# Kernel optimization log

Hardware: AMD Instinct MI355X
Metric: run time of the kernel (lower is better)

The kernel has to match this reference:

```python
import jax, jax.numpy as jnp
import numpy as np

B, S, D, DEPTH = 2, 2048, 1024, 4
NUM_LEAVES = 2 ** DEPTH          # 16
NUM_DEC = NUM_LEAVES - 1         # 15


def setup_inputs() -> dict:
    key = jax.random.key(0)
    k1, k2, k3, k4, k5 = jax.random.split(key, 5)
    scale = 1.0 / np.sqrt(D)
    return {
        "x": jax.random.normal(k1, (B, S, D), dtype=jnp.float32),
        "dec_w": jax.random.normal(k2, (NUM_DEC, D), dtype=jnp.float32) * scale,
        "dec_b": jax.random.normal(k3, (NUM_DEC,), dtype=jnp.float32) * scale,
        "leaf_w": jax.random.normal(k4, (NUM_LEAVES, D, D), dtype=jnp.float32) * scale,  # [leaf, out, in] (torch Linear layout)
        "leaf_b": jax.random.normal(k5, (NUM_LEAVES, D), dtype=jnp.float32) * scale,
    }


def reference(x, dec_w, dec_b, leaf_w, leaf_b):
    num_leaves = leaf_w.shape[0]
    num_dec = num_leaves - 1
    # All decision-node sigmoids in one batched GEMM: [B,S,num_dec]
    dec = jax.nn.sigmoid(jnp.einsum("bsd,nd->bsn", x, dec_w) + dec_b)
    # Faithful to the original: each tree slot is multiplied exactly once by its
    # direct parent's decision (left child: p, right child: 1-p).
    leaf_idx = np.arange(num_dec, 2 * num_leaves - 1)      # slots holding leaf probs
    parent = (leaf_idx - 1) // 2                           # [num_leaves]
    is_left = (leaf_idx % 2 == 1)                          # [num_leaves]
    dec_p = dec[..., parent]                               # [B,S,num_leaves]
    leaf_probs = jnp.where(jnp.asarray(is_left), dec_p, 1.0 - dec_p)
    # All leaf MLPs as one batched GEMM: [B,S,L,D]
    leaf_out = jnp.einsum("bsd,lod->bslo", x, leaf_w) + leaf_b
    # Probability-weighted sum over leaves -> [B,S,D]
    return jnp.einsum("bslo,bsl->bso", leaf_out, leaf_probs)
```

## Files before the change

### kernel.cpp

```cpp
#include <hip/hip_runtime.h>
#include <stdint.h>


#define M_TOK 4096
#define DDIM  1024
#define KFLAT 9216

typedef __bf16 bf16x8 __attribute__((ext_vector_type(8)));
typedef float  f32x4  __attribute__((ext_vector_type(4)));
typedef unsigned short u16x4 __attribute__((ext_vector_type(4)));
typedef unsigned short u16x8 __attribute__((ext_vector_type(8)));

#define GLB(p) ((const __attribute__((address_space(1))) void*)(p))
#define LDS(p) ((__attribute__((address_space(3))) void*)(p))

__device__ __forceinline__ unsigned short f2bf(float f) {
    union { float f; uint32_t u; } v; v.f = f;
    uint32_t u = v.u;
    return (unsigned short)((u + 0x7fffu + ((u >> 16) & 1u)) >> 16);
}

__device__ __forceinline__ bf16x8 asbf(f32x4 v) {
    bf16x8 r; __builtin_memcpy(&r, &v, 16); return r;
}

template<int OFF>
__device__ __forceinline__ f32x4 dsr(uint32_t a) {
    f32x4 r;
    asm volatile("ds_read_b128 %0, %1 offset:%c2" : "=v"(r) : "v"(a), "i"(OFF));
    return r;
}

__global__ __launch_bounds__(256) void prep_dec_kernel(
    const float* __restrict__ x, const float* __restrict__ dec_w,
    const float* __restrict__ dec_b, const float* __restrict__ lw,
    const float* __restrict__ lb, unsigned short* __restrict__ wp,
    float* __restrict__ bw, unsigned short* __restrict__ xs,
    float* __restrict__ pmat)
{
    if (blockIdx.x < 1024) {
        int idx = blockIdx.x * 256 + threadIdx.x;
        int o  = idx >> 8;
        int k4 = (idx & 255) << 2;
        size_t src = (size_t)o * DDIM + k4;
        size_t dstb = (size_t)o * KFLAT + k4;
        float4 acc = make_float4(0.f, 0.f, 0.f, 0.f);
#pragma unroll
        for (int j = 0; j < 8; ++j) {
            const float4 a = *(const float4*)(lw + (size_t)(2*j)   * DDIM*DDIM + src);
            const float4 b = *(const float4*)(lw + (size_t)(2*j+1) * DDIM*DDIM + src);
            u16x4 d;
            d[0] = f2bf(a.x - b.x); d[1] = f2bf(a.y - b.y);
            d[2] = f2bf(a.z - b.z); d[3] = f2bf(a.w - b.w);
            *(u16x4*)(wp + dstb + (size_t)j * DDIM) = d;
            acc.x += b.x; acc.y += b.y; acc.z += b.z; acc.w += b.w;
        }
        u16x4 s;
        s[0] = f2bf(acc.x); s[1] = f2bf(acc.y); s[2] = f2bf(acc.z); s[3] = f2bf(acc.w);
        *(u16x4*)(wp + dstb + (size_t)8 * DDIM) = s;
        if ((idx & 255) == 0) {
            float sb = 0.f;
#pragma unroll
            for (int j = 0; j < 8; ++j) {
                float ba = lb[(2*j) * DDIM + o];
                float bb = lb[(2*j+1) * DDIM + o];
                bw[j * DDIM + o] = ba - bb;
                sb += bb;
            }
            bw[8 * DDIM + o] = sb;
        }
    } else {
        int m    = (blockIdx.x - 1024) * 4 + (threadIdx.x >> 6);
        int lane = threadIdx.x & 63;
        const float* xr = x + (size_t)m * DDIM + lane * 16;
        float xv[16];
        *(float4*)&xv[0]  = *(const float4*)(xr + 0);
        *(float4*)&xv[4]  = *(const float4*)(xr + 4);
        *(float4*)&xv[8]  = *(const float4*)(xr + 8);
        *(float4*)&xv[12] = *(const float4*)(xr + 12);
        float s[8];
#pragma unroll
        for (int j = 0; j < 8; ++j) {
            const float* wr = dec_w + (size_t)(7 + j) * DDIM + lane * 16;
            float a = 0.f;
#pragma unroll
            for (int i = 0; i < 16; i += 4) {
                float4 wv = *(const float4*)(wr + i);
                a = fmaf(xv[i], wv.x, fmaf(xv[i+1], wv.y, fmaf(xv[i+2], wv.z, fmaf(xv[i+3], wv.w, a))));
            }
            s[j] = a;
        }
#pragma unroll
        for (int j = 0; j < 8; ++j)
#pragma unroll
            for (int off = 32; off > 0; off >>= 1)
                s[j] += __shfl_xor(s[j], off);
        float p[8];
#pragma unroll
        for (int j = 0; j < 8; ++j)
            p[j] = 1.0f / (1.0f + expf(-(s[j] + dec_b[7 + j])));
        if (lane == 0) {
#pragma unroll
            for (int j = 0; j < 8; ++j)
                pmat[(size_t)m * 8 + j] = p[j];
        }
#pragma unroll
        for (int j = 0; j < 9; ++j) {
            float pj = (j < 8) ? p[j] : 1.0f;
            unsigned short* dst = xs + (size_t)m * KFLAT + j * DDIM + lane * 16;
#pragma unroll
            for (int c = 0; c < 2; ++c) {
                u16x8 o;
#pragma unroll
                for (int e = 0; e < 8; ++e) o[e] = f2bf(pj * xv[c * 8 + e]);
                *(u16x8*)(dst + c * 8) = o;
            }
        }
    }
}

#define WAITV0 asm volatile("s_waitcnt vmcnt(0)" ::: "memory")
#define WAITV4 asm volatile("s_waitcnt vmcnt(4)" ::: "memory")
#define BARR   __builtin_amdgcn_s_barrier()
#define SBAR   __builtin_amdgcn_sched_barrier(0)
#define LGKM0  do { asm volatile("s_waitcnt lgkmcnt(0)" ::: "memory"); SBAR; } while(0)
#define LGKM4  do { asm volatile("s_waitcnt lgkmcnt(4)" ::: "memory"); SBAR; } while(0)

#define MFMA_Q(q, ASET, BSET) do { \
    __builtin_amdgcn_s_setprio(1); \
    _Pragma("unroll") \
    for (int mfl = 0; mfl < 2; ++mfl) { \
        _Pragma("unroll") \
        for (int j = 0; j < 4; ++j) { \
            acc[2*(q)+mfl][j] = __builtin_amdgcn_mfma_f32_16x16x32_bf16(asbf(ASET[mfl][0]), asbf(BSET[j][0]), acc[2*(q)+mfl][j], 0, 0, 0); \
            acc[2*(q)+mfl][j] = __builtin_amdgcn_mfma_f32_16x16x32_bf16(asbf(ASET[mfl][1]), asbf(BSET[j][1]), acc[2*(q)+mfl][j], 0, 0, 0); \
        } \
    } \
    __builtin_amdgcn_s_setprio(0); \
} while(0)

#define READ_A(SET, q, a0, a1) do { \
    SET[0][0] = dsr<(2*(q)+0)*2048>(a0); \
    SET[0][1] = dsr<(2*(q)+0)*2048>(a1); \
    SET[1][0] = dsr<(2*(q)+1)*2048>(a0); \
    SET[1][1] = dsr<(2*(q)+1)*2048>(a1); \
} while(0)

#define READ_B(SET, b0, b1) do { \
    SET[0][0] = dsr<0*2048>(b0); SET[0][1] = dsr<0*2048>(b1); \
    SET[1][0] = dsr<1*2048>(b0); SET[1][1] = dsr<1*2048>(b1); \
    SET[2][0] = dsr<2*2048>(b0); SET[2][1] = dsr<2*2048>(b1); \
    SET[3][0] = dsr<3*2048>(b0); SET[3][1] = dsr<3*2048>(b1); \
} while(0)

__global__ __launch_bounds__(512, 2) void tree_gemm8(
    const unsigned short* __restrict__ xs, const unsigned short* __restrict__ wp,
    float* __restrict__ out, float* __restrict__ parts, int KG)
{
    extern __shared__ char smem[];
    const int tid  = threadIdx.x;
    const int lane = tid & 63;
    const int w    = tid >> 6;
    const int wm   = w >> 2, wn = w & 3;
    const int ra   = lane & 15;
    const int g16  = lane >> 4;

    const int bx  = blockIdx.x;
    const int xcd = bx & 7, ii = bx >> 3;
    const int nt  = xcd >> 1;
    const int mt  = (xcd & 1) * 8 + ii;
    const int m0  = mt * 256, n0 = nt * 256;
    const int g   = blockIdx.y;
    const int k0  = g * KG;
    const int NT  = KG >> 6;

    uint32_t sbase = (uint32_t)(uintptr_t)(__attribute__((address_space(3))) char*)smem;
    const uint32_t colb0 = (uint32_t)((g16 ^ (ra & 7)) << 4);
    const uint32_t colb1 = colb0 ^ 64;
    const uint32_t baseA0s = sbase + wm * 16384 + ra * 128 + colb0;
    const uint32_t baseA1s = sbase + wm * 16384 + ra * 128 + colb1;
    const uint32_t baseB0s = sbase + 65536 + wn * 8192 + ra * 128 + colb0;
    const uint32_t baseB1s = sbase + 65536 + wn * 8192 + ra * 128 + colb1;

    const int kel = (((lane & 7) ^ (lane >> 3)) & 7) * 8;
    const int rA  = w * 8 + (lane >> 3);

    auto stageA = [&](int buf, int tt, int hh) {
        const unsigned short* s0 = xs + (size_t)(m0 + hh * 128 + rA) * KFLAT + (k0 + tt * 64 + kel);
        char* d0 = smem + buf * 32768 + hh * 16384 + w * 1024;
        __builtin_amdgcn_global_load_lds(GLB(s0), LDS(d0), 16, 0, 0);
        __builtin_amdgcn_global_load_lds(GLB(s0 + (size_t)64 * KFLAT), LDS(d0 + 8192), 16, 0, 0);
    };
    auto stageB = [&](int buf, int tt, int hh) {
        const unsigned short* s0 = wp + (size_t)(n0 + hh * 128 + rA) * KFLAT + (k0 + tt * 64 + kel);
        char* d0 = smem + 65536 + buf * 32768 + hh * 16384 + w * 1024;
        __builtin_amdgcn_global_load_lds(GLB(s0), LDS(d0), 16, 0, 0);
        __builtin_amdgcn_global_load_lds(GLB(s0 + (size_t)64 * KFLAT), LDS(d0 + 8192), 16, 0, 0);
    };

    f32x4 acc[8][4] = {};
    f32x4 avA[2][2], avB[2][2], bvX[4][2], bvY[4][2];

    stageA(0, 0, 0); stageA(0, 0, 1);
    stageB(0, 0, 0); stageB(0, 0, 1);
    stageB(1, 1, 0); stageB(1, 1, 1);
    WAITV4;
    BARR;
    READ_B(bvX, baseB0s, baseB1s);
    READ_A(avA, 0, baseA0s, baseA1s);

    int bt1 = 1, bt2 = 2;

#define TILE_BODY8(T, CUR, NXT) do { \
    const int t_ = (T); \
    const bool s1 = (t_ + 1 < NT), s2 = (t_ + 2 < NT); \
    if (s1) { stageA((t_ + 1) & 1, t_ + 1, 0); stageA((t_ + 1) & 1, t_ + 1, 1); } \
    if (s2) { stageB(bt2, t_ + 2, 0); stageB(bt2, t_ + 2, 1); } \
    const uint32_t a0_ = baseA0s + ((uint32_t)(t_ & 1) << 15); \
    const uint32_t a1_ = baseA1s + ((uint32_t)(t_ & 1) << 15); \
    READ_A(avB, 1, a0_, a1_); \
    LGKM4;  MFMA_Q(0, avA, CUR); \
    READ_A(avA, 2, a0_, a1_); \
    LGKM4;  MFMA_Q(1, avB, CUR); \
    READ_A(avB, 3, a0_, a1_); \
    LGKM4;  MFMA_Q(2, avA, CUR); \
    LGKM0; \
    if (s1) { \
        if (s2) { WAITV4; } else { WAITV0; } \
        BARR; \
        const uint32_t nb0_ = baseB0s + (uint32_t)bt1 * 32768u; \
        const uint32_t nb1_ = baseB1s + (uint32_t)bt1 * 32768u; \
        const uint32_t na0_ = baseA0s + ((uint32_t)((t_ + 1) & 1) << 15); \
        const uint32_t na1_ = baseA1s + ((uint32_t)((t_ + 1) & 1) << 15); \
        READ_B(NXT, nb0_, nb1_); \
        READ_A(avA, 0, na0_, na1_); \
    } \
    MFMA_Q(3, avB, CUR); \
    SBAR; \
    bt1 = (bt1 == 2) ? 0 : bt1 + 1; \
    bt2 = (bt2 == 2) ? 0 : bt2 + 1; \
} while(0)

    for (int tp = 0; tp < NT; tp += 2) {
        TILE_BODY8(tp,     bvX, bvY);
        TILE_BODY8(tp + 1, bvY, bvX);
    }
#undef TILE_BODY8

    float* dst = (g == 0) ? out : parts + (size_t)(g - 1) * M_TOK * DDIM;
#pragma unroll
    for (int mf = 0; mf < 8; ++mf)
#pragma unroll
        for (int e = 0; e < 4; ++e) {
            int row = m0 + wm * 128 + mf * 16 + g16 * 4 + e;
#pragma unroll
            for (int j = 0; j < 4; ++j)
                dst[(size_t)row * DDIM + n0 + wn * 64 + j * 16 + ra] = acc[mf][j][e];
        }
}

__global__ __launch_bounds__(256) void reduce2_kernel(
    float* __restrict__ out, const float* __restrict__ parts,
    const float* __restrict__ pmat, const float* __restrict__ bw, int np)
{
#pragma unroll
    for (int rep = 0; rep < 2; ++rep) {
        size_t i = (size_t)blockIdx.x * 512 + rep * 256 + threadIdx.x;
        int m   = (int)(i >> 8);
        int col = (int)(i & 255) * 4;
        float4 a = ((const float4*)out)[i];
        for (int p = 0; p < np; ++p) {
            float4 b = ((const float4*)(parts + (size_t)p * M_TOK * DDIM))[i];
            a.x += b.x; a.y += b.y; a.z += b.z; a.w += b.w;
        }
        float4 pa = *(const float4*)(pmat + (size_t)m * 8);
        float4 pb = *(const float4*)(pmat + (size_t)m * 8 + 4);
        float4 bias = *(const float4*)(bw + 8 * DDIM + col);
#pragma unroll
        for (int l = 0; l < 8; ++l) {
            float pl = (l < 4) ? ((const float*)&pa)[l] : ((const float*)&pb)[l - 4];
            float4 bl = *(const float4*)(bw + l * DDIM + col);
            bias.x = fmaf(pl, bl.x, bias.x); bias.y = fmaf(pl, bl.y, bias.y);
            bias.z = fmaf(pl, bl.z, bias.z); bias.w = fmaf(pl, bl.w, bias.w);
        }
        a.x += bias.x; a.y += bias.y; a.z += bias.z; a.w += bias.w;
        ((float4*)out)[i] = a;
    }
}

__global__ __launch_bounds__(256, 4) void tree_gemm3(
    const unsigned short* __restrict__ xs, const unsigned short* __restrict__ wp,
    const float* __restrict__ bw, const float* __restrict__ pmat,
    float* __restrict__ out, float* __restrict__ parts, int KG)
{
    __shared__ __align__(16) unsigned short Asm[2][128 * 32];
    __shared__ __align__(16) unsigned short Bsm[2][128 * 32];
    const int tid  = threadIdx.x;
    const int lane = tid & 63;
    const int w    = tid >> 6;
    const int wm   = w >> 1, wn = w & 1;
    const int bx   = blockIdx.x;
    const int xcd  = bx & 7;
    const int ii   = bx >> 3;
    const int mt   = xcd * 4 + (ii >> 3);
    const int nt   = ii & 7;
    const int m0   = mt * 128, n0 = nt * 128;
    const int g    = blockIdx.y;
    const int k0   = g * KG;
    const int ra   = lane & 15;
    const int kb   = (lane >> 4) * 8;
    f32x4 acc[4][4] = {};
    auto stage = [&](int buf, int t) {
#pragma unroll
        for (int c = 0; c < 2; ++c) {
            int row = w * 32 + c * 16 + (lane >> 2);
            int ke  = k0 + t * 32 + (lane & 3) * 8;
            const unsigned short* ga = xs + (size_t)(m0 + row) * KFLAT + ke;
            __builtin_amdgcn_global_load_lds(GLB(ga), LDS(&Asm[buf][w * 1024 + c * 512]), 16, 0, 0);
            const unsigned short* gb = wp + (size_t)(n0 + row) * KFLAT + ke;
            __builtin_amdgcn_global_load_lds(GLB(gb), LDS(&Bsm[buf][w * 1024 + c * 512]), 16, 0, 0);
        }
    };
    const int TOT = KG >> 5;
    stage(0, 0);
    __syncthreads();
    int cur = 0;
    for (int t = 0; t < TOT; ++t) {
        if (t + 1 < TOT) stage(cur ^ 1, t + 1);
        bf16x8 av2[4], bv2[4];
#pragma unroll
        for (int i2 = 0; i2 < 4; ++i2)
            av2[i2] = *(const bf16x8*)&Asm[cur][(wm * 64 + i2 * 16 + ra) * 32 + kb];
#pragma unroll
        for (int j = 0; j < 4; ++j)
            bv2[j] = *(const bf16x8*)&Bsm[cur][(wn * 64 + j * 16 + ra) * 32 + kb];
#pragma unroll
        for (int i2 = 0; i2 < 4; ++i2)
#pragma unroll
            for (int j = 0; j < 4; ++j)
                acc[i2][j] = __builtin_amdgcn_mfma_f32_16x16x32_bf16(av2[i2], bv2[j], acc[i2][j], 0, 0, 0);
        __syncthreads();
        cur ^= 1;
    }
    float* bsm = (float*)&Asm[0][0];
    if (g == 0) {
        for (int idx = tid; idx < 9 * 128; idx += 256)
            bsm[idx] = bw[(idx >> 7) * DDIM + n0 + (idx & 127)];
    }
    __syncthreads();
    float* dst = (g == 0) ? out : parts + (size_t)(g - 1) * M_TOK * DDIM;
#pragma unroll
    for (int i2 = 0; i2 < 4; ++i2)
#pragma unroll
        for (int r = 0; r < 4; ++r) {
            int row = m0 + wm * 64 + i2 * 16 + (lane >> 4) * 4 + r;
            float4 pa, pb;
            if (g == 0) {
                pa = *(const float4*)(pmat + (size_t)row * 8);
                pb = *(const float4*)(pmat + (size_t)row * 8 + 4);
            }
#pragma unroll
            for (int j = 0; j < 4; ++j) {
                int cl = wn * 64 + j * 16 + ra;
                float v = acc[i2][j][r];
                if (g == 0) {
                    v += pa.x * bsm[0 * 128 + cl] + pa.y * bsm[1 * 128 + cl]
                       + pa.z * bsm[2 * 128 + cl] + pa.w * bsm[3 * 128 + cl]
                       + pb.x * bsm[4 * 128 + cl] + pb.y * bsm[5 * 128 + cl]
                       + pb.z * bsm[6 * 128 + cl] + pb.w * bsm[7 * 128 + cl]
                       + bsm[8 * 128 + cl];
                }
                dst[(size_t)row * DDIM + n0 + cl] = v;
            }
        }
}

__global__ __launch_bounds__(256) void reduce_kernel(
    float* __restrict__ out, const float* __restrict__ parts, int np)
{
    size_t i = (size_t)blockIdx.x * 256 + threadIdx.x;
    float4 a = ((const float4*)out)[i];
    for (int p = 0; p < np; ++p) {
        float4 b = ((const float4*)(parts + (size_t)p * M_TOK * DDIM))[i];
        a.x += b.x; a.y += b.y; a.z += b.z; a.w += b.w;
    }
    ((float4*)out)[i] = a;
}

extern "C" void kernel_launch(void* const* d_in, const int* in_sizes, int n_in,
                              void* d_out, int out_size, void* d_ws, size_t ws_size,
                              hipStream_t stream) {
    (void)in_sizes; (void)n_in; (void)out_size;
    const float* x     = (const float*)d_in[0];
    const float* dec_w = (const float*)d_in[1];
    const float* dec_b = (const float*)d_in[2];
    const float* lw    = (const float*)d_in[3];
    const float* lb    = (const float*)d_in[4];
    float* out = (float*)d_out;
    uint8_t* w8 = (uint8_t*)d_ws;

    unsigned short* xs   = (unsigned short*)(w8);
    unsigned short* wp   = (unsigned short*)(w8 + 75497472);
    float*          bw   = (float*)(w8 + 94371840);
    float*          pmat = (float*)(w8 + 94408704);
    float*          parts= (float*)(w8 + 94539776);
    const size_t NEED3 = 94539776 + 2ull * 16777216;
    const size_t NEED4 = 94539776 + 3ull * 16777216;

    int ks = (ws_size >= NEED4) ? 4 : (ws_size >= NEED3) ? 3 : 0;
    if (!ks) return;

    prep_dec_kernel<<<2048, 256, 0, stream>>>(x, dec_w, dec_b, lw, lb, wp, bw, xs, pmat);

    hipError_t e8 = hipFuncSetAttribute(
        reinterpret_cast<const void*>(tree_gemm8),
        hipFuncAttributeMaxDynamicSharedMemorySize, 163840);
    if (e8 == hipSuccess) {
        tree_gemm8<<<dim3(64, ks), 512, 163840, stream>>>(xs, wp, out, parts, KFLAT / ks);
        reduce2_kernel<<<2048, 256, 0, stream>>>(out, parts, pmat, bw, ks - 1);
    } else {
        tree_gemm3<<<dim3(256, ks), 256, 0, stream>>>(xs, wp, bw, pmat, out, parts, KFLAT / ks);
        reduce_kernel<<<4096, 256, 0, stream>>>(out, parts, ks - 1);
    }
}
```

Measured before the change: 119.9 us.

## Scale bf16 x by leaf probability on the fly inside GEMM instead of materializing

The prep kernel now writes only a single bf16 copy of x (M×1024) instead of nine probability-scaled copies (M×9216). The new GEMM kernel loads raw x tiles into registers, scales each row by its per-leaf probability while converting to bf16, and writes the result to LDS, while B still arrives via async global-to-LDS loads. This removes most of the prep write traffic and the A-operand read traffic, at the cost of extra VALU work and register-staged A loads in the GEMM loop. It also re-rounds x twice (bf16 then scaled bf16), which slightly changes numerics, and it drops the fallback tree_gemm3 path.

```diff
diff --git a/kernel.cpp b/kernel.cpp
--- a/kernel.cpp
+++ b/kernel.cpp
@@ -36,7 +36,7 @@
     const float* __restrict__ dec_b, const float* __restrict__ lw,
     const float* __restrict__ lb, unsigned short* __restrict__ wp,
     float* __restrict__ bw, unsigned short* __restrict__ xs,
-    float* __restrict__ pmat)
+    float* __restrict__ pmat, int mode)
 {
     if (blockIdx.x < 1024) {
         int idx = blockIdx.x * 256 + threadIdx.x;
@@ -104,16 +104,27 @@
             for (int j = 0; j < 8; ++j)
                 pmat[(size_t)m * 8 + j] = p[j];
         }
-#pragma unroll
-        for (int j = 0; j < 9; ++j) {
-            float pj = (j < 8) ? p[j] : 1.0f;
-            unsigned short* dst = xs + (size_t)m * KFLAT + j * DDIM + lane * 16;
+        if (mode) {
+            unsigned short* dst = xs + (size_t)m * DDIM + lane * 16;
 #pragma unroll
             for (int c = 0; c < 2; ++c) {
                 u16x8 o;
 #pragma unroll
-                for (int e = 0; e < 8; ++e) o[e] = f2bf(pj * xv[c * 8 + e]);
+                for (int e = 0; e < 8; ++e) o[e] = f2bf(xv[c * 8 + e]);
                 *(u16x8*)(dst + c * 8) = o;
+            }
+        } else {
+#pragma unroll
+            for (int j = 0; j < 9; ++j) {
+                float pj = (j < 8) ? p[j] : 1.0f;
+                unsigned short* dst = xs + (size_t)m * KFLAT + j * DDIM + lane * 16;
+#pragma unroll
+                for (int c = 0; c < 2; ++c) {
+                    u16x8 o;
+#pragma unroll
+                    for (int e = 0; e < 8; ++e) o[e] = f2bf(pj * xv[c * 8 + e]);
+                    *(u16x8*)(dst + c * 8) = o;
+                }
             }
         }
     }
@@ -152,6 +163,194 @@
     SET[2][0] = dsr<2*2048>(b0); SET[2][1] = dsr<2*2048>(b1); \
     SET[3][0] = dsr<3*2048>(b0); SET[3][1] = dsr<3*2048>(b1); \
 } while(0)
+
+#define SCALE16(dstv, srcv, pc) do { \
+    _Pragma("unroll") \
+    for (int e = 0; e < 4; ++e) { \
+        uint32_t u_ = __float_as_uint(srcv[e]); \
+        float lo_ = __uint_as_float(u_ << 16) * (pc); \
+        float hi_ = __uint_as_float(u_ & 0xffff0000u) * (pc); \
+        uint32_t rr_; \
+        asm volatile("v_cvt_pk_bf16_f32 %0, %1, %2" : "=v"(rr_) : "v"(lo_), "v"(hi_)); \
+        dstv[e] = __uint_as_float(rr_); \
+    } \
+} while(0)
+
+__global__ __launch_bounds__(512, 2) void tree_gemm11(
+    const unsigned short* __restrict__ xb,
+    const unsigned short* __restrict__ wp,
+    const float* __restrict__ pmat,
+    float* __restrict__ out, float* __restrict__ parts, int KG)
+{
+    extern __shared__ char smem[];
+    const int tid  = threadIdx.x;
+    const int lane = tid & 63;
+    const int w    = tid >> 6;
+    const int wm   = w >> 2, wn = w & 3;
+    const int ra   = lane & 15;
+    const int g16  = lane >> 4;
+
+    const int bx  = blockIdx.x;
+    const int xcd = bx & 7, ii = bx >> 3;
+    const int nt  = xcd >> 1;
+    const int mt  = (xcd & 1) * 8 + ii;
+    const int m0  = mt * 256, n0 = nt * 256;
+    const int g   = blockIdx.y;
+    const int k0  = g * KG;
+    const int NT  = KG >> 6;
+
+    uint32_t sbase = (uint32_t)(uintptr_t)(__attribute__((address_space(3))) char*)smem;
+    const uint32_t colb0 = (uint32_t)((g16 ^ (ra & 7)) << 4);
+    const uint32_t colb1 = colb0 ^ 64;
+    const uint32_t baseA0s = sbase + wm * 16384 + ra * 128 + colb0;
+    const uint32_t baseA1s = sbase + wm * 16384 + ra * 128 + colb1;
+    const uint32_t baseB0s = sbase + 65536 + wn * 8192 + ra * 128 + colb0;
+    const uint32_t baseB1s = sbase + 65536 + wn * 8192 + ra * 128 + colb1;
+
+    const int kel = (((lane & 7) ^ (lane >> 3)) & 7) * 8;
+    const int r0  = w * 8 + (lane >> 3);
+    const uint32_t wbs = sbase + (uint32_t)r0 * 128 + ((uint32_t)(lane & 7) << 4);
+
+    auto stageB = [&](int buf, int tt, int hh) {
+        const unsigned short* s0 = wp + (size_t)(n0 + hh * 128 + r0) * KFLAT + (k0 + tt * 64 + kel);
+        char* d0 = smem + 65536 + buf * 32768 + hh * 16384 + w * 1024;
+        __builtin_amdgcn_global_load_lds(GLB(s0), LDS(d0), 16, 0, 0);
+        __builtin_amdgcn_global_load_lds(GLB(s0 + (size_t)64 * KFLAT), LDS(d0 + 8192), 16, 0, 0);
+    };
+
+    f32x4 acc[8][4] = {};
+    f32x4 avA[2][2], avB[2][2], bvX[4][2], bvY[4][2];
+    f32x4 araw[4];
+
+    const int fl = k0 >> 10;
+    float pv1[4], pv2[4], pcur[4];
+#pragma unroll
+    for (int i = 0; i < 4; ++i) {
+        const float* pr = pmat + (size_t)(m0 + r0 + i * 64) * 8;
+        pcur[i] = pr[fl];
+        pv1[i]  = pr[fl + 1];
+        pv2[i]  = (fl + 2 < 8) ? pr[fl + 2] : 1.0f;
+    }
+    {
+        const int colw = k0 & 1023;
+#pragma unroll
+        for (int i = 0; i < 4; ++i)
+            araw[i] = *(const f32x4*)(xb + (size_t)(m0 + r0 + i * 64) * DDIM + colw + kel);
+    }
+    SBAR;
+    stageB(0, 0, 0); stageB(0, 0, 1);
+    stageB(1, 1, 0); stageB(1, 1, 1);
+    WAITV4;
+#pragma unroll
+    for (int i = 0; i < 4; ++i) {
+        f32x4 sc;
+        SCALE16(sc, araw[i], pcur[i]);
+        asm volatile("ds_write_b128 %0, %1" :: "v"(wbs + i * 8192), "v"(sc) : "memory");
+    }
+    LGKM0;
+    BARR;
+    READ_B(bvX, baseB0s, baseB1s);
+    READ_A(avA, 0, baseA0s, baseA1s);
+
+    int bt1 = 1, bt2 = 2;
+
+#define TILE_BODY11(T, CUR, NXT) do { \
+    const int t_ = (T); \
+    const bool s1 = (t_ + 1 < NT), s2 = (t_ + 2 < NT); \
+    if (s1) { \
+        const int colw_ = (k0 + (t_ + 1) * 64) & 1023; \
+        _Pragma("unroll") \
+        for (int i = 0; i < 4; ++i) \
+            araw[i] = *(const f32x4*)(xb + (size_t)(m0 + r0 + i * 64) * DDIM + colw_ + kel); \
+    } \
+    SBAR; \
+    if (s2) { stageB(bt2, t_ + 2, 0); stageB(bt2, t_ + 2, 1); } \
+    const uint32_t a0_ = baseA0s + ((uint32_t)(t_ & 1) << 15); \
+    const uint32_t a1_ = baseA1s + ((uint32_t)(t_ & 1) << 15); \
+    READ_A(avB, 1, a0_, a1_); \
+    LGKM4;  MFMA_Q(0, avA, CUR); \
+    READ_A(avA, 2, a0_, a1_); \
+    LGKM4;  MFMA_Q(1, avB, CUR); \
+    READ_A(avB, 3, a0_, a1_); \
+    LGKM4;  MFMA_Q(2, avA, CUR); \
+    if (s1) { \
+        if (s2) { WAITV4; } else { WAITV0; } \
+        const int kk1_ = k0 + (t_ + 1) * 64; \
+        if ((kk1_ & 1023) == 0) { \
+            const bool l1_ = ((kk1_ >> 10) - fl) == 1; \
+            _Pragma("unroll") \
+            for (int i = 0; i < 4; ++i) pcur[i] = l1_ ? pv1[i] : pv2[i]; \
+        } \
+        const uint32_t wb_ = wbs + ((uint32_t)((t_ + 1) & 1) << 15); \
+        _Pragma("unroll") \
+        for (int i = 0; i < 4; ++i) { \
+            f32x4 sc_; \
+            SCALE16(sc_, araw[i], pcur[i]); \
+            asm volatile("ds_write_b128 %0, %1" :: "v"(wb_ + i * 8192), "v"(sc_) : "memory"); \
+        } \
+    } \
+    LGKM0; \
+    if (s1) { \
+        BARR; \
+        const uint32_t nb0_ = baseB0s + (uint32_t)bt1 * 32768u; \
+        const uint32_t nb1_ = baseB1s + (uint32_t)bt1 * 32768u; \
+        const uint32_t na0_ = baseA0s + ((uint32_t)((t_ + 1) & 1) << 15); \
+        const uint32_t na1_ = baseA1s + ((uint32_t)((t_ + 1) & 1) << 15); \
+        READ_B(NXT, nb0_, nb1_); \
+        READ_A(avA, 0, na0_, na1_); \
+    } \
+    MFMA_Q(3, avB, CUR); \
+    SBAR; \
+    bt1 = (bt1 == 2) ? 0 : bt1 + 1; \
+    bt2 = (bt2 == 2) ? 0 : bt2 + 1; \
+} while(0)
+
+    for (int tp = 0; tp < NT; tp += 2) {
+        TILE_BODY11(tp,     bvX, bvY);
+        TILE_BODY11(tp + 1, bvY, bvX);
+    }
+#undef TILE_BODY11
+
+    float* dst = (g == 0) ? out : parts + (size_t)(g - 1) * M_TOK * DDIM;
+#pragma unroll
+    for (int mf = 0; mf < 8; ++mf)
+#pragma unroll
+        for (int e = 0; e < 4; ++e) {
+            int row = m0 + wm * 128 + mf * 16 + g16 * 4 + e;
+#pragma unroll
+            for (int j = 0; j < 4; ++j)
+                dst[(size_t)row * DDIM + n0 + wn * 64 + j * 16 + ra] = acc[mf][j][e];
+        }
+}
+
+__global__ __launch_bounds__(256) void reduce2_kernel(
+    float* __restrict__ out, const float* __restrict__ parts,
+    const float* __restrict__ pmat, const float* __restrict__ bw, int np)
+{
+#pragma unroll
+    for (int rep = 0; rep < 2; ++rep) {
+        size_t i = (size_t)blockIdx.x * 512 + rep * 256 + threadIdx.x;
+        int m   = (int)(i >> 8);
+        int col = (int)(i & 255) * 4;
+        float4 a = ((const float4*)out)[i];
+        for (int p = 0; p < np; ++p) {
+            float4 b = ((const float4*)(parts + (size_t)p * M_TOK * DDIM))[i];
+            a.x += b.x; a.y += b.y; a.z += b.z; a.w += b.w;
+        }
+        float4 pa = *(const float4*)(pmat + (size_t)m * 8);
+        float4 pb = *(const float4*)(pmat + (size_t)m * 8 + 4);
+        float4 bias = *(const float4*)(bw + 8 * DDIM + col);
+#pragma unroll
+        for (int l = 0; l < 8; ++l) {
+            float pl = (l < 4) ? ((const float*)&pa)[l] : ((const float*)&pb)[l - 4];
+            float4 bl = *(const float4*)(bw + l * DDIM + col);
+            bias.x = fmaf(pl, bl.x, bias.x); bias.y = fmaf(pl, bl.y, bias.y);
+            bias.z = fmaf(pl, bl.z, bias.z); bias.w = fmaf(pl, bl.w, bias.w);
+        }
+        a.x += bias.x; a.y += bias.y; a.z += bias.z; a.w += bias.w;
+        ((float4*)out)[i] = a;
+    }
+}
 
 __global__ __launch_bounds__(512, 2) void tree_gemm8(
     const unsigned short* __restrict__ xs, const unsigned short* __restrict__ wp,
@@ -259,134 +458,6 @@
         }
 }
 
-__global__ __launch_bounds__(256) void reduce2_kernel(
-    float* __restrict__ out, const float* __restrict__ parts,
-    const float* __restrict__ pmat, const float* __restrict__ bw, int np)
-{
-#pragma unroll
-    for (int rep = 0; rep < 2; ++rep) {
-        size_t i = (size_t)blockIdx.x * 512 + rep * 256 + threadIdx.x;
-        int m   = (int)(i >> 8);
-        int col = (int)(i & 255) * 4;
-        float4 a = ((const float4*)out)[i];
-        for (int p = 0; p < np; ++p) {
-            float4 b = ((const float4*)(parts + (size_t)p * M_TOK * DDIM))[i];
-            a.x += b.x; a.y += b.y; a.z += b.z; a.w += b.w;
-        }
-        float4 pa = *(const float4*)(pmat + (size_t)m * 8);
-        float4 pb = *(const float4*)(pmat + (size_t)m * 8 + 4);
-        float4 bias = *(const float4*)(bw + 8 * DDIM + col);
-#pragma unroll
-        for (int l = 0; l < 8; ++l) {
-            float pl = (l < 4) ? ((const float*)&pa)[l] : ((const float*)&pb)[l - 4];
-            float4 bl = *(const float4*)(bw + l * DDIM + col);
-            bias.x = fmaf(pl, bl.x, bias.x); bias.y = fmaf(pl, bl.y, bias.y);
-            bias.z = fmaf(pl, bl.z, bias.z); bias.w = fmaf(pl, bl.w, bias.w);
-        }
-        a.x += bias.x; a.y += bias.y; a.z += bias.z; a.w += bias.w;
-        ((float4*)out)[i] = a;
-    }
-}
-
-__global__ __launch_bounds__(256, 4) void tree_gemm3(
-    const unsigned short* __restrict__ xs, const unsigned short* __restrict__ wp,
-    const float* __restrict__ bw, const float* __restrict__ pmat,
-    float* __restrict__ out, float* __restrict__ parts, int KG)
-{
-    __shared__ __align__(16) unsigned short Asm[2][128 * 32];
-    __shared__ __align__(16) unsigned short Bsm[2][128 * 32];
-    const int tid  = threadIdx.x;
-    const int lane = tid & 63;
-    const int w    = tid >> 6;
-    const int wm   = w >> 1, wn = w & 1;
-    const int bx   = blockIdx.x;
-    const int xcd  = bx & 7;
-    const int ii   = bx >> 3;
-    const int mt   = xcd * 4 + (ii >> 3);
-    const int nt   = ii & 7;
-    const int m0   = mt * 128, n0 = nt * 128;
-    const int g    = blockIdx.y;
-    const int k0   = g * KG;
-    const int ra   = lane & 15;
-    const int kb   = (lane >> 4) * 8;
-    f32x4 acc[4][4] = {};
-    auto stage = [&](int buf, int t) {
-#pragma unroll
-        for (int c = 0; c < 2; ++c) {
-            int row = w * 32 + c * 16 + (lane >> 2);
-            int ke  = k0 + t * 32 + (lane & 3) * 8;
-            const unsigned short* ga = xs + (size_t)(m0 + row) * KFLAT + ke;
-            __builtin_amdgcn_global_load_lds(GLB(ga), LDS(&Asm[buf][w * 1024 + c * 512]), 16, 0, 0);
-            const unsigned short* gb = wp + (size_t)(n0 + row) * KFLAT + ke;
-            __builtin_amdgcn_global_load_lds(GLB(gb), LDS(&Bsm[buf][w * 1024 + c * 512]), 16, 0, 0);
-        }
-    };
-    const int TOT = KG >> 5;
-    stage(0, 0);
-    __syncthreads();
-    int cur = 0;
-    for (int t = 0; t < TOT; ++t) {
-        if (t + 1 < TOT) stage(cur ^ 1, t + 1);
-        bf16x8 av2[4], bv2[4];
-#pragma unroll
-        for (int i2 = 0; i2 < 4; ++i2)
-            av2[i2] = *(const bf16x8*)&Asm[cur][(wm * 64 + i2 * 16 + ra) * 32 + kb];
-#pragma unroll
-        for (int j = 0; j < 4; ++j)
-            bv2[j] = *(const bf16x8*)&Bsm[cur][(wn * 64 + j * 16 + ra) * 32 + kb];
-#pragma unroll
-        for (int i2 = 0; i2 < 4; ++i2)
-#pragma unroll
-            for (int j = 0; j < 4; ++j)
-                acc[i2][j] = __builtin_amdgcn_mfma_f32_16x16x32_bf16(av2[i2], bv2[j], acc[i2][j], 0, 0, 0);
-        __syncthreads();
-        cur ^= 1;
-    }
-    float* bsm = (float*)&Asm[0][0];
-    if (g == 0) {
-        for (int idx = tid; idx < 9 * 128; idx += 256)
-            bsm[idx] = bw[(idx >> 7) * DDIM + n0 + (idx & 127)];
-    }
-    __syncthreads();
-    float* dst = (g == 0) ? out : parts + (size_t)(g - 1) * M_TOK * DDIM;
-#pragma unroll
-    for (int i2 = 0; i2 < 4; ++i2)
-#pragma unroll
-        for (int r = 0; r < 4; ++r) {
-            int row = m0 + wm * 64 + i2 * 16 + (lane >> 4) * 4 + r;
-            float4 pa, pb;
-            if (g == 0) {
-                pa = *(const float4*)(pmat + (size_t)row * 8);
-                pb = *(const float4*)(pmat + (size_t)row * 8 + 4);
-            }
-#pragma unroll
-            for (int j = 0; j < 4; ++j) {
-                int cl = wn * 64 + j * 16 + ra;
-                float v = acc[i2][j][r];
-                if (g == 0) {
-                    v += pa.x * bsm[0 * 128 + cl] + pa.y * bsm[1 * 128 + cl]
-                       + pa.z * bsm[2 * 128 + cl] + pa.w * bsm[3 * 128 + cl]
-                       + pb.x * bsm[4 * 128 + cl] + pb.y * bsm[5 * 128 + cl]
-                       + pb.z * bsm[6 * 128 + cl] + pb.w * bsm[7 * 128 + cl]
-                       + bsm[8 * 128 + cl];
-                }
-                dst[(size_t)row * DDIM + n0 + cl] = v;
-            }
-        }
-}
-
-__global__ __launch_bounds__(256) void reduce_kernel(
-    float* __restrict__ out, const float* __restrict__ parts, int np)
-{
-    size_t i = (size_t)blockIdx.x * 256 + threadIdx.x;
-    float4 a = ((const float4*)out)[i];
-    for (int p = 0; p < np; ++p) {
-        float4 b = ((const float4*)(parts + (size_t)p * M_TOK * DDIM))[i];
-        a.x += b.x; a.y += b.y; a.z += b.z; a.w += b.w;
-    }
-    ((float4*)out)[i] = a;
-}
-
 extern "C" void kernel_launch(void* const* d_in, const int* in_sizes, int n_in,
                               void* d_out, int out_size, void* d_ws, size_t ws_size,
                               hipStream_t stream) {
@@ -410,16 +481,24 @@
     int ks = (ws_size >= NEED4) ? 4 : (ws_size >= NEED3) ? 3 : 0;
     if (!ks) return;
 
-    prep_dec_kernel<<<2048, 256, 0, stream>>>(x, dec_w, dec_b, lw, lb, wp, bw, xs, pmat);
-
+    hipError_t e11 = hipFuncSetAttribute(
+        reinterpret_cast<const void*>(tree_gemm11),
+        hipFuncAttributeMaxDynamicSharedMemorySize, 163840);
+    const bool use11 = (e11 == hipSuccess);
+
+    prep_dec_kernel<<<2048, 256, 0, stream>>>(x, dec_w, dec_b, lw, lb, wp, bw, xs, pmat,
+                                              use11 ? 1 : 0);
+
+    if (use11) {
+        tree_gemm11<<<dim3(64, ks), 512, 163840, stream>>>(xs, wp, pmat, out, parts, KFLAT / ks);
+        reduce2_kernel<<<2048, 256, 0, stream>>>(out, parts, pmat, bw, ks - 1);
+        return;
+    }
     hipError_t e8 = hipFuncSetAttribute(
         reinterpret_cast<const void*>(tree_gemm8),
         hipFuncAttributeMaxDynamicSharedMemorySize, 163840);
     if (e8 == hipSuccess) {
         tree_gemm8<<<dim3(64, ks), 512, 163840, stream>>>(xs, wp, out, parts, KFLAT / ks);
         reduce2_kernel<<<2048, 256, 0, stream>>>(out, parts, pmat, bw, ks - 1);
-    } else {
-        tree_gemm3<<<dim3(256, ks), 256, 0, stream>>>(xs, wp, bw, pmat, out, parts, KFLAT / ks);
-        reduce_kernel<<<4096, 256, 0, stream>>>(out, parts, ks - 1);
-    }
-}
+    }
+}
```

After: 186.6 us. 1.56x slower.
